# Kernel tuning notes

Measured on AMD Instinct MI355X. Metric: run time of the kernel, lower is better.

## Reference

```python
import jax, jax.numpy as jnp
import numpy as np

L = 4          # n_layers
HID = 64       # hidden_channels
MODES = 16     # n_modes
HEADS = 4      # n_heads
NP_SP = 500    # spatial engram patterns
NP_FR = 200    # spectral engram patterns
ED = 8         # embed_dim
WS = 4         # spatial window size
PRIME = 31.0


def setup_inputs() -> dict:
    key = jax.random.key(0)
    ks = jax.random.split(key, 20)
    B, Cin, Cout, S = 16, 3, 1, 16384
    f = lambda k, sh: jax.random.normal(k, sh, dtype=jnp.float32) * 0.05
    ch = HID // HEADS
    return {
        "x": jax.random.normal(ks[0], (B, Cin, S), dtype=jnp.float32),
        "lift_W": f(ks[1], (Cin, HID)), "lift_b": f(ks[2], (HID,)),
        "proj_W": f(ks[3], (HID, Cout)), "proj_b": f(ks[4], (Cout,)),
        "sp_emb": f(ks[5], (L, NP_SP, ED)), "sp_W": f(ks[6], (L, ED, HID)), "sp_b": f(ks[7], (L, HID)),
        "fr_emb": f(ks[8], (L, NP_FR, ED)), "fr_W": f(ks[9], (L, ED, HID * MODES)), "fr_b": f(ks[10], (L, HID * MODES)),
        "g_W1": f(ks[11], (L, 3 * HID, 64)), "g_b1": f(ks[12], (L, 64)),
        "g_W2": f(ks[13], (L, 64, 3)), "g_b2": f(ks[14], (L, 3)),
        "mhf_Wr": f(ks[15], (L, HEADS, ch, ch, MODES)),
        "mhf_Wi": f(ks[16], (L, HEADS, ch, ch, MODES)),
    }


def _spatial_engram(x, emb, W, b):
    # x: [B, C, S] -> hash each replicate-padded window of size WS -> embedding gather -> linear
    B, C, S = x.shape
    pad = WS // 2
    xp = jnp.pad(x, ((0, 0), (0, 0), (pad, pad)), mode='edge')   # [B, C, S+WS]
    sC = xp.sum(axis=1)                                          # [B, S+WS]
    # window sum over WS consecutive positions (vectorized over all seq positions)
    wsum = sC[:, 0:S] + sC[:, 1:S + 1] + sC[:, 2:S + 2] + sC[:, 3:S + 3]  # [B, S]
    idx = (wsum * PRIME).astype(jnp.int32) % NP_SP               # truncate-toward-zero like torch .long()
    idx = jnp.clip(idx, 0, NP_SP - 1)
    e = emb[idx]                                                 # [B, S, ED] gather
    out = e @ W + b                                              # [B, S, C]
    return out.transpose(0, 2, 1)                                # [B, C, S]


def _spectral_engram(x, emb, W, b):
    B, C, S = x.shape
    xf = jnp.fft.rfft(x, axis=-1)                                # [B, C, F]
    mag = jnp.abs(xf[:, :, :MODES]).mean(axis=1)                 # [B, MODES]
    idx = ((mag * 1000.0).astype(jnp.int32)).sum(axis=1) % NP_FR # [B]
    e = emb[idx]                                                 # [B, ED]
    proj = (e @ W + b).reshape(B, C, MODES)
    full = jnp.zeros((B, C, xf.shape[-1]), dtype=xf.dtype).at[:, :, :MODES].set(proj.astype(xf.dtype))
    return jnp.fft.irfft(full, n=S, axis=-1)


def _mhf_spectral_conv(x, Wr, Wi):
    # multi-head Fourier spectral conv: per-head complex channel mixing on low modes
    B, C, S = x.shape
    ch = C // HEADS
    xf = jnp.fft.rfft(x, axis=-1)                                # [B, C, F]
    xh = xf[:, :, :MODES].reshape(B, HEADS, ch, MODES)           # [B, H, ch, M]
    Wc = Wr + 1j * Wi                                            # [H, ch, ch, M]
    of = jnp.einsum('bhim,hiom->bhom', xh, Wc).reshape(B, C, MODES)
    full = jnp.zeros((B, C, xf.shape[-1]), dtype=xf.dtype).at[:, :, :MODES].set(of)
    return jnp.fft.irfft(full, n=S, axis=-1)


def _gated_fusion(sp, mh, fr, W1, b1, W2, b2):
    g = jnp.concatenate([sp.mean(-1), mh.mean(-1), fr.mean(-1)], axis=-1)  # [B, 3C]
    h = jax.nn.relu(g @ W1 + b1)
    w = jax.nn.softmax(h @ W2 + b2, axis=-1)                     # [B, 3]
    return (w[:, 0, None, None] * sp + w[:, 1, None, None] * mh + w[:, 2, None, None] * fr)


def reference(x, lift_W, lift_b, proj_W, proj_b, sp_emb, sp_W, sp_b,
              fr_emb, fr_W, fr_b, g_W1, g_b1, g_W2, g_b2, mhf_Wr, mhf_Wi):
    # lifting: [B, Cin, S] -> [B, HID, S]
    h = jnp.einsum('bcs,cd->bds', x, lift_W) + lift_b[None, :, None]
    for i in range(L):
        sp = _spatial_engram(h, sp_emb[i], sp_W[i], sp_b[i])
        mh = _mhf_spectral_conv(h, mhf_Wr[i], mhf_Wi[i])
        fr = _spectral_engram(h, fr_emb[i], fr_W[i], fr_b[i])
        h = _gated_fusion(sp, mh, fr, g_W1[i], g_b1[i], g_W2[i], g_b2[i])
        h = jax.nn.gelu(h, approximate=False)  # torch F.gelu default = exact erf
    out = jnp.einsum('bcs,cd->bds', h, proj_W) + proj_b[None, :, None]
    return out
```

## Files before the change

kernel.cpp:

```cpp
#include <hip/hip_runtime.h>
#include <math.h>

#define B_ 16
#define CIN_ 3
#define HID_ 64
#define S_ 16384
#define MODES_ 16
#define HEADS_ 4
#define CH_ 16
#define ED_ 8
#define NPSP_ 500
#define NPFR_ 200
#define LAYERS_ 4
#define RECW_ 42

__device__ __forceinline__ double gelu_exact(double v) {
    double y = v * 0.70710678118654752440;
    double t = y * y;
    double p = -1.2290555301717926e-09;
    p = fma(p, t, 1.4807192815879218e-08);
    p = fma(p, t, -1.6365838718281893e-07);
    p = fma(p, t, 1.6462114365889246e-06);
    p = fma(p, t, -1.4925650358406251e-05);
    p = fma(p, t, 1.2055332981789664e-04);
    p = fma(p, t, -8.5483270234508528e-04);
    p = fma(p, t, 5.2239776254421878e-03);
    p = fma(p, t, -2.6866170645131252e-02);
    p = fma(p, t, 1.1283791670955126e-01);
    p = fma(p, t, -3.7612638903183752e-01);
    p = fma(p, t, 1.1283791670955126e+00);
    double er = y * p;
    if (t > 0.5000001) er = erf(y);
    return 0.5 * v * (1.0 + er);
}

__device__ __constant__ double KC_[16] = {1.0, 0.99518472667219688624,
    0.98078528040323044913, 0.95694033573220886494, 0.92387953251128675613,
    0.88192126434835502971, 0.83146961230254523708, 0.77301045336273696081,
    0.70710678118654752440, 0.63439328416364549822, 0.55557023301960222474,
    0.47139673682599764856, 0.38268343236508977173, 0.29028467725446236764,
    0.19509032201612826785, 0.09801714032956060199};
__device__ __constant__ double KS_[16] = {0.0, 0.09801714032956060199,
    0.19509032201612826785, 0.29028467725446236764, 0.38268343236508977173,
    0.47139673682599764856, 0.55557023301960222474, 0.63439328416364549822,
    0.70710678118654752440, 0.77301045336273696081, 0.83146961230254523708,
    0.88192126434835502971, 0.92387953251128675613, 0.95694033573220886494,
    0.98078528040323044913, 0.99518472667219688624};

__global__ __launch_bounds__(256) void k_lift(const float* __restrict__ x,
                                              const float* __restrict__ W,
                                              const float* __restrict__ bias,
                                              float* __restrict__ h,
                                              double* __restrict__ sC2) {
    int b = blockIdx.y;
    int s = blockIdx.x * 256 + threadIdx.x;
    const float* xb = x + (size_t)b * CIN_ * S_ + s;
    double x0 = (double)xb[0];
    double x1 = (double)xb[S_];
    double x2 = (double)xb[2 * S_];
    float* hb = h + (size_t)b * HID_ * S_ + s;
    double accA = 0.0, accB = 0.0;
    for (int d = 0; d < HID_; ++d) {
        double v = x0 * (double)W[d];
        v = fma(x1, (double)W[HID_ + d], v);
        v = fma(x2, (double)W[2 * HID_ + d], v);
        v += (double)bias[d];
        hb[(size_t)d * S_] = (float)v;
        if (d < 32) accA += v; else accB += v;
    }
    sC2[(size_t)b * S_ + s] = accA;
    sC2[(size_t)(B_ + b) * S_ + s] = accB;
}

__global__ __launch_bounds__(256) void k_hash(const double* __restrict__ sC2,
                                              const float* __restrict__ emb_l,
                                              int* __restrict__ idx,
                                              double* __restrict__ Eb) {
    int b = blockIdx.y;
    int s0 = blockIdx.x * 256;
    int t = threadIdx.x;
    __shared__ double sl[260];
    for (int j = t; j < 260; j += 256) {
        int p = s0 - 2 + j;
        p = p < 0 ? 0 : (p > S_ - 1 ? S_ - 1 : p);
        sl[j] = sC2[(size_t)b * S_ + p] + sC2[(size_t)(B_ + b) * S_ + p];
    }
    __syncthreads();
    double wsum = ((sl[t] + sl[t + 1]) + sl[t + 2]) + sl[t + 3];
    int ti = (int)(wsum * 31.0);
    int id = ti % NPSP_;
    if (id < 0) id += NPSP_;
    idx[(size_t)b * S_ + s0 + t] = id;

    const float* er = emb_l + id * ED_;
    double ev[8];
#pragma unroll
    for (int k = 0; k < 8; k++) ev[k] = (double)er[k];

    int lane = t & 63, wv = t >> 6;
    __shared__ double red[4][8];
#pragma unroll
    for (int k = 0; k < 8; k++) {
        double v = ev[k];
        for (int off = 32; off > 0; off >>= 1) v += __shfl_down(v, off, 64);
        if (lane == 0) red[wv][k] = v;
    }
    __syncthreads();
    if (t < 8) {
        double v = red[0][t] + red[1][t] + red[2][t] + red[3][t];
        atomicAdd(&Eb[b * ED_ + t], v);
    }
}

__global__ __launch_bounds__(256, 2) void k_dft(const float* __restrict__ h,
                                                double* __restrict__ Xr,
                                                double* __restrict__ Xi) {
    int b = blockIdx.y;
    int c0 = blockIdx.x * 2;
    int t = threadIdx.x;
    const float* h0 = h + ((size_t)(b * HID_ + c0)) * S_ + t;
    const float* h1 = h0 + S_;

    double acc[64];
#pragma unroll
    for (int k = 0; k < 64; k++) acc[k] = 0.0;

    double cmv[16], smv[16];
    cmv[0] = 1.0; smv[0] = 0.0;
    cmv[1] = cospi((double)t / 8192.0);
    smv[1] = sinpi((double)t / 8192.0);
#pragma unroll
    for (int m = 2; m < 16; m++) {
        cmv[m] = cmv[m - 1] * cmv[1] - smv[m - 1] * smv[1];
        smv[m] = smv[m - 1] * cmv[1] + cmv[m - 1] * smv[1];
    }

    for (int k = 0; k < 16; k++) {
        int s = k << 8;
        double a0 = (double)h0[s];
        double b0 = (double)h0[s + 4096];
        double c0v = (double)h0[s + 8192];
        double d0 = (double)h0[s + 12288];
        double a1 = (double)h1[s];
        double b1 = (double)h1[s + 4096];
        double c1v = (double)h1[s + 8192];
        double d1 = (double)h1[s + 12288];

        double t10 = a0 + c0v, t20 = b0 + d0;
        double g00 = t10 + t20, g20 = t10 - t20;
        double ar0 = a0 - c0v, br0 = b0 - d0;
        double t11 = a1 + c1v, t21 = b1 + d1;
        double g01 = t11 + t21, g21 = t11 - t21;
        double ar1 = a1 - c1v, br1 = b1 - d1;

        acc[0] += g00;
        acc[32] += g01;
#pragma unroll
        for (int m = 1; m < 16; m++) {
            double c = cmv[m], s_ = smv[m];
            if ((m & 1) == 0) {
                double g0x = (m & 2) ? g20 : g00;
                double g1x = (m & 2) ? g21 : g01;
                acc[m]      = fma(g0x, c,  acc[m]);
                acc[16 + m] = fma(g0x, s_, acc[16 + m]);
                acc[32 + m] = fma(g1x, c,  acc[32 + m]);
                acc[48 + m] = fma(g1x, s_, acc[48 + m]);
            } else if ((m & 2) == 0) {
                acc[m]      = fma(ar0, c,  fma(-br0, s_, acc[m]));
                acc[16 + m] = fma(ar0, s_, fma( br0, c,  acc[16 + m]));
                acc[32 + m] = fma(ar1, c,  fma(-br1, s_, acc[32 + m]));
                acc[48 + m] = fma(ar1, s_, fma( br1, c,  acc[48 + m]));
            } else {
                acc[m]      = fma(ar0, c,  fma( br0, s_, acc[m]));
                acc[16 + m] = fma(ar0, s_, fma(-br0, c,  acc[16 + m]));
                acc[32 + m] = fma(ar1, c,  fma( br1, s_, acc[32 + m]));
                acc[48 + m] = fma(ar1, s_, fma(-br1, c,  acc[48 + m]));
            }
        }
#pragma unroll
        for (int m = 1; m < 16; m++) {
            double cn = cmv[m] * KC_[m] - smv[m] * KS_[m];
            double sn = smv[m] * KC_[m] + cmv[m] * KS_[m];
            cmv[m] = cn; smv[m] = sn;
        }
    }

    int lane = t & 63, wv = t >> 6;
    __shared__ double red[4][64];
#pragma unroll
    for (int k = 0; k < 64; k++) {
        double v = acc[k];
        for (int off = 32; off > 0; off >>= 1) v += __shfl_down(v, off, 64);
        if (lane == 0) red[wv][k] = v;
    }
    __syncthreads();
    if (t < 64) {
        double v = red[0][t] + red[1][t] + red[2][t] + red[3][t];
        int cc = t >> 5, im = (t >> 4) & 1, m = t & 15;
        size_t o = ((size_t)b * HID_ + c0 + cc) * MODES_ + m;
        if (im) Xi[o] = -v;
        else    Xr[o] = v;
    }
}

__global__ __launch_bounds__(256) void k_gate(const double* __restrict__ Xr,
                                              const double* __restrict__ Xi,
                                              const float* __restrict__ mWr,
                                              const float* __restrict__ mWi,
                                              const float* __restrict__ fr_emb_l,
                                              const float* __restrict__ fr_W_l,
                                              const float* __restrict__ fr_b_l,
                                              const double* __restrict__ Eb,
                                              const float* __restrict__ sp_W_l,
                                              const float* __restrict__ sp_b_l,
                                              const float* __restrict__ gW1,
                                              const float* __restrict__ gb1,
                                              const float* __restrict__ gW2,
                                              const float* __restrict__ gb2,
                                              double* __restrict__ RECg) {
    int b = blockIdx.x;
    int t = threadIdx.x;
    __shared__ double sXr[1024], sXi[1024];
    __shared__ double sMr[1024], sMi[1024], sP[1024];
    __shared__ double gg[192], h1s[64], sww[3];
    __shared__ int magI[MODES_];
    __shared__ int fidxS;

    for (int j = t; j < 1024; j += 256) {
        sXr[j] = Xr[(size_t)b * 1024 + j];
        sXi[j] = Xi[(size_t)b * 1024 + j];
    }
    __syncthreads();

    if (t < MODES_) {
        double acc = 0.0;
        for (int c = 0; c < HID_; c++) {
            double re = sXr[c * MODES_ + t];
            double im = sXi[c * MODES_ + t];
            acc += sqrt(re * re + im * im);
        }
        magI[t] = (int)(acc * (1.0 / 64.0) * 1000.0);
    }

    for (int u = t; u < 1024; u += 256) {
        int hh = u >> 8, rem = u & 255, o = rem >> 4, m = rem & 15;
        const float* wr = mWr + (size_t)hh * CH_ * CH_ * MODES_;
        const float* wi = mWi + (size_t)hh * CH_ * CH_ * MODES_;
        double aR = 0.0, aI = 0.0;
#pragma unroll 4
        for (int i = 0; i < CH_; i++) {
            double xrv = sXr[(hh * CH_ + i) * MODES_ + m];
            double xiv = sXi[(hh * CH_ + i) * MODES_ + m];
            double wrv = (double)wr[(i * CH_ + o) * MODES_ + m];
            double wiv = (double)wi[(i * CH_ + o) * MODES_ + m];
            aR += xrv * wrv - xiv * wiv;
            aI += xrv * wiv + xiv * wrv;
        }
        sMr[(hh * CH_ + o) * MODES_ + m] = aR;
        sMi[(hh * CH_ + o) * MODES_ + m] = aI;
    }
    __syncthreads();

    if (t == 0) {
        int ssum = 0;
        for (int m = 0; m < MODES_; m++) ssum += magI[m];
        int f = ssum % NPFR_;
        if (f < 0) f += NPFR_;
        fidxS = f;
    }
    __syncthreads();

    {
        const float* fe = fr_emb_l + fidxS * ED_;
        for (int u = t; u < 1024; u += 256) {
            double acc = 0.0;
            for (int e = 0; e < ED_; e++)
                acc += (double)fe[e] * (double)fr_W_l[e * 1024 + u];
            sP[u] = acc + (double)fr_b_l[u];
        }
    }
    __syncthreads();

    if (t < 64) {
        double a = 0.0;
        for (int e = 0; e < ED_; e++)
            a += Eb[b * ED_ + e] * (double)sp_W_l[e * 64 + t];
        gg[t]       = a * (1.0 / 16384.0) + (double)sp_b_l[t];
        gg[64 + t]  = sMr[t * MODES_] * (1.0 / 16384.0);
        gg[128 + t] = sP[t * MODES_] * (1.0 / 16384.0);
    }
    __syncthreads();
    if (t < 64) {
        double a = 0.0;
        for (int k = 0; k < 192; k++) a += gg[k] * (double)gW1[k * 64 + t];
        a += (double)gb1[t];
        h1s[t] = a > 0.0 ? a : 0.0;
    }
    __syncthreads();
    if (t == 0) {
        double l[3];
        for (int j = 0; j < 3; j++) {
            double a = 0.0;
            for (int k = 0; k < 64; k++) a += h1s[k] * (double)gW2[k * 3 + j];
            l[j] = a + (double)gb2[j];
        }
        double mx = fmax(l[0], fmax(l[1], l[2]));
        double e0 = exp(l[0] - mx), e1 = exp(l[1] - mx), e2 = exp(l[2] - mx);
        double sum = e0 + e1 + e2;
        sww[0] = e0 / sum; sww[1] = e1 / sum; sww[2] = e2 / sum;
    }
    __syncthreads();

    double w0s = sww[0], w1s = sww[1], w2s = sww[2];
    double* R = RECg + (size_t)b * HID_ * RECW_;
    for (int u = t; u < 1024; u += 256) {
        int c = u >> 4, m = u & 15;
        double km = (m == 0 ? 1.0 : 2.0) * (1.0 / 16384.0);
        R[c * RECW_ + 2 * m]     = km * (w1s * sMr[u] + w2s * sP[u]);
        R[c * RECW_ + 2 * m + 1] = (m == 0) ? 0.0 : -(km * w1s * sMi[u]);
    }
    for (int u = t; u < 512; u += 256) {
        int e = u >> 6, c = u & 63;
        R[c * RECW_ + 32 + e] = w0s * (double)sp_W_l[u];
    }
    if (t < 64) {
        R[t * RECW_ + 40] = w0s * (double)sp_b_l[t];
        R[t * RECW_ + 41] = 0.0;
    }
}

__global__ __launch_bounds__(256, 2) void k_recon(const int* __restrict__ idx,
                                                  const float* __restrict__ sp_emb_l,
                                                  const double* __restrict__ RECg,
                                                  float* __restrict__ h,
                                                  double* __restrict__ sC2) {
    int b = blockIdx.y;
    int cz = blockIdx.z;
    int cbase = cz * 32;
    int s0 = blockIdx.x * 256 + threadIdx.x;
    int t = threadIdx.x;
    __shared__ double rec[32 * RECW_];
    __shared__ float semb[NPSP_ * 9];
    for (int j = t; j < 32 * RECW_; j += 256)
        rec[j] = RECg[(size_t)b * HID_ * RECW_ + cbase * RECW_ + j];
    for (int j4 = t; j4 < NPSP_ * 2; j4 += 256) {
        float4 v = reinterpret_cast<const float4*>(sp_emb_l)[j4];
        int r = j4 >> 1, e0 = (j4 & 1) * 4;
        semb[r * 9 + e0]     = v.x;
        semb[r * 9 + e0 + 1] = v.y;
        semb[r * 9 + e0 + 2] = v.z;
        semb[r * 9 + e0 + 3] = v.w;
    }
    __syncthreads();

    int id0 = idx[(size_t)b * S_ + s0];
    int id1 = idx[(size_t)b * S_ + s0 + 4096];
    int id2 = idx[(size_t)b * S_ + s0 + 8192];
    int id3 = idx[(size_t)b * S_ + s0 + 12288];
    double e0v[8], e1v[8], e2v[8], e3v[8];
#pragma unroll
    for (int k = 0; k < 8; k++) {
        e0v[k] = (double)semb[id0 * 9 + k];
        e1v[k] = (double)semb[id1 * 9 + k];
        e2v[k] = (double)semb[id2 * 9 + k];
        e3v[k] = (double)semb[id3 * 9 + k];
    }

    double cb = cospi((double)s0 / 8192.0);
    double sb = sinpi((double)s0 / 8192.0);
    double cm[16], sm[16];
    cm[0] = 1.0; sm[0] = 0.0;
    cm[1] = cb;  sm[1] = sb;
#pragma unroll
    for (int m = 2; m < 16; m++) {
        cm[m] = cm[m - 1] * cb - sm[m - 1] * sb;
        sm[m] = sm[m - 1] * cb + cm[m - 1] * sb;
    }

    float* hb = h + (size_t)b * HID_ * S_ + (size_t)cbase * S_;
    double cs0 = 0.0, cs1 = 0.0, cs2 = 0.0, cs3 = 0.0;
    for (int c = 0; c < 32; c++) {
        const double2* r2 = (const double2*)(rec + c * RECW_);
        double base = rec[c * RECW_ + 40];
        double p0 = base, p1 = base, p2 = base, p3 = base;
#pragma unroll
        for (int k = 0; k < 4; k++) {
            double2 w = r2[16 + k];
            p0 = fma(e0v[2 * k], w.x, p0); p0 = fma(e0v[2 * k + 1], w.y, p0);
            p1 = fma(e1v[2 * k], w.x, p1); p1 = fma(e1v[2 * k + 1], w.y, p1);
            p2 = fma(e2v[2 * k], w.x, p2); p2 = fma(e2v[2 * k + 1], w.y, p2);
            p3 = fma(e3v[2 * k], w.x, p3); p3 = fma(e3v[2 * k + 1], w.y, p3);
        }
        double PA = 0.0, PB = 0.0, PC = 0.0, PD = 0.0, QB = 0.0, QD = 0.0;
#pragma unroll
        for (int mm = 0; mm < 16; mm += 4) {
            double2 q0 = r2[mm], q1 = r2[mm + 1], q2 = r2[mm + 2], q3 = r2[mm + 3];
            PA = fma(q0.x, cm[mm], PA);     PA = fma(q0.y, sm[mm], PA);
            PB = fma(q1.x, cm[mm + 1], PB); PB = fma(q1.y, sm[mm + 1], PB);
            QB = fma(q1.y, cm[mm + 1], QB); QB = fma(-q1.x, sm[mm + 1], QB);
            PC = fma(q2.x, cm[mm + 2], PC); PC = fma(q2.y, sm[mm + 2], PC);
            PD = fma(q3.x, cm[mm + 3], PD); PD = fma(q3.y, sm[mm + 3], PD);
            QD = fma(q3.y, cm[mm + 3], QD); QD = fma(-q3.x, sm[mm + 3], QD);
        }
        double u0 = PA + PC, u1 = PA - PC;
        double w0 = PB + PD, qd = QB - QD;
        double g0 = gelu_exact(p0 + (u0 + w0));
        double g1 = gelu_exact(p1 + (u1 + qd));
        double g2 = gelu_exact(p2 + (u0 - w0));
        double g3 = gelu_exact(p3 + (u1 - qd));
        hb[(size_t)c * S_ + s0]         = (float)g0;
        hb[(size_t)c * S_ + s0 + 4096]  = (float)g1;
        hb[(size_t)c * S_ + s0 + 8192]  = (float)g2;
        hb[(size_t)c * S_ + s0 + 12288] = (float)g3;
        cs0 += g0; cs1 += g1; cs2 += g2; cs3 += g3;
    }
    double* sc = sC2 + (size_t)(cz * B_ + b) * S_;
    sc[s0]         = cs0;
    sc[s0 + 4096]  = cs1;
    sc[s0 + 8192]  = cs2;
    sc[s0 + 12288] = cs3;
}

__global__ __launch_bounds__(256) void k_proj(const float* __restrict__ h,
                                              const float* __restrict__ pW,
                                              const float* __restrict__ pb,
                                              float* __restrict__ out) {
    int b = blockIdx.y;
    int s = blockIdx.x * 256 + threadIdx.x;
    const float* hb = h + (size_t)b * HID_ * S_ + s;
    double acc = 0.0;
    for (int d = 0; d < HID_; d++)
        acc += (double)hb[(size_t)d * S_] * (double)pW[d];
    out[(size_t)b * S_ + s] = (float)(acc + (double)pb[0]);
}

extern "C" void kernel_launch(void* const* d_in, const int* in_sizes, int n_in,
                              void* d_out, int out_size, void* d_ws, size_t ws_size,
                              hipStream_t stream) {
    const float* x      = (const float*)d_in[0];
    const float* lift_W = (const float*)d_in[1];
    const float* lift_b = (const float*)d_in[2];
    const float* proj_W = (const float*)d_in[3];
    const float* proj_b = (const float*)d_in[4];
    const float* sp_emb = (const float*)d_in[5];
    const float* sp_W   = (const float*)d_in[6];
    const float* sp_b   = (const float*)d_in[7];
    const float* fr_emb = (const float*)d_in[8];
    const float* fr_W   = (const float*)d_in[9];
    const float* fr_b   = (const float*)d_in[10];
    const float* g_W1   = (const float*)d_in[11];
    const float* g_b1   = (const float*)d_in[12];
    const float* g_W2   = (const float*)d_in[13];
    const float* g_b2   = (const float*)d_in[14];
    const float* mhf_Wr = (const float*)d_in[15];
    const float* mhf_Wi = (const float*)d_in[16];

    char* ws = (char*)d_ws;
    float* h    = (float*)ws;   ws += (size_t)B_ * HID_ * S_ * 4;
    double* sC2 = (double*)ws;  ws += (size_t)2 * B_ * S_ * 8;
    int* idx    = (int*)ws;     ws += (size_t)B_ * S_ * 4;
    double* Xr  = (double*)ws;  ws += (size_t)B_ * HID_ * MODES_ * 8;
    double* Xi  = (double*)ws;  ws += (size_t)B_ * HID_ * MODES_ * 8;
    double* REC = (double*)ws;  ws += (size_t)B_ * HID_ * RECW_ * 8;
    double* Eb  = (double*)ws;  ws += (size_t)LAYERS_ * B_ * ED_ * 8;

    hipMemsetAsync(Eb, 0, (size_t)LAYERS_ * B_ * ED_ * 8, stream);

    dim3 blk(256);
    k_lift<<<dim3(S_ / 256, B_), blk, 0, stream>>>(x, lift_W, lift_b, h, sC2);

    for (int lay = 0; lay < LAYERS_; ++lay) {
        k_hash<<<dim3(S_ / 256, B_), blk, 0, stream>>>(
            sC2, sp_emb + (size_t)lay * NPSP_ * ED_, idx, Eb + (size_t)lay * B_ * ED_);
        k_dft<<<dim3(HID_ / 2, B_), blk, 0, stream>>>(h, Xr, Xi);
        k_gate<<<dim3(B_), blk, 0, stream>>>(
            Xr, Xi,
            mhf_Wr + (size_t)lay * HEADS_ * CH_ * CH_ * MODES_,
            mhf_Wi + (size_t)lay * HEADS_ * CH_ * CH_ * MODES_,
            fr_emb + (size_t)lay * NPFR_ * ED_,
            fr_W + (size_t)lay * ED_ * HID_ * MODES_,
            fr_b + (size_t)lay * HID_ * MODES_,
            Eb + (size_t)lay * B_ * ED_,
            sp_W + (size_t)lay * ED_ * HID_,
            sp_b + (size_t)lay * HID_,
            g_W1 + (size_t)lay * 192 * 64,
            g_b1 + (size_t)lay * 64,
            g_W2 + (size_t)lay * 64 * 3,
            g_b2 + (size_t)lay * 3,
            REC);
        k_recon<<<dim3(S_ / 1024, B_, 2), blk, 0, stream>>>(
            idx, sp_emb + (size_t)lay * NPSP_ * ED_, REC, h, sC2);
    }

    k_proj<<<dim3(S_ / 256, B_), blk, 0, stream>>>(h, proj_W, proj_b, (float*)d_out);
}
```

Measured before the change: 569.0 us.

## Fuse hash into DFT kernel and split recon over four channel groups

Merges the spatial hash kernel into the DFT kernel as extra blocks in the same grid, so the two independent stages share one launch and run concurrently. The recon kernel now handles 16 channels per block across four z-slices instead of 32 across two, doubling its parallelism. Channel partial sums grow from two to four planes, so the hash step reads four buffers instead of two. The recon blocks now load the full embedding table into shared memory for half as many channels each, which adds redundant loads in exchange for more blocks.

After: 623.7 us. 1.1x slower.

```diff
diff --git a/kernel.cpp b/kernel.cpp
--- a/kernel.cpp
+++ b/kernel.cpp
@@ -51,7 +51,7 @@
                                               const float* __restrict__ W,
                                               const float* __restrict__ bias,
                                               float* __restrict__ h,
-                                              double* __restrict__ sC2) {
+                                              double* __restrict__ sC4) {
     int b = blockIdx.y;
     int s = blockIdx.x * 256 + threadIdx.x;
     const float* xb = x + (size_t)b * CIN_ * S_ + s;
@@ -59,147 +59,153 @@
     double x1 = (double)xb[S_];
     double x2 = (double)xb[2 * S_];
     float* hb = h + (size_t)b * HID_ * S_ + s;
-    double accA = 0.0, accB = 0.0;
+    double accs[4] = {0.0, 0.0, 0.0, 0.0};
     for (int d = 0; d < HID_; ++d) {
         double v = x0 * (double)W[d];
         v = fma(x1, (double)W[HID_ + d], v);
         v = fma(x2, (double)W[2 * HID_ + d], v);
         v += (double)bias[d];
         hb[(size_t)d * S_] = (float)v;
-        if (d < 32) accA += v; else accB += v;
-    }
-    sC2[(size_t)b * S_ + s] = accA;
-    sC2[(size_t)(B_ + b) * S_ + s] = accB;
-}
-
-__global__ __launch_bounds__(256) void k_hash(const double* __restrict__ sC2,
-                                              const float* __restrict__ emb_l,
-                                              int* __restrict__ idx,
-                                              double* __restrict__ Eb) {
+        accs[d >> 4] += v;
+    }
+#pragma unroll
+    for (int z = 0; z < 4; z++)
+        sC4[(size_t)(z * B_ + b) * S_ + s] = accs[z];
+}
+
+__global__ __launch_bounds__(256, 2) void k_dfthash(const float* __restrict__ h,
+                                                    double* __restrict__ Xr,
+                                                    double* __restrict__ Xi,
+                                                    const double* __restrict__ sC4,
+                                                    const float* __restrict__ emb_l,
+                                                    int* __restrict__ idx,
+                                                    double* __restrict__ Eb) {
     int b = blockIdx.y;
-    int s0 = blockIdx.x * 256;
     int t = threadIdx.x;
-    __shared__ double sl[260];
-    for (int j = t; j < 260; j += 256) {
-        int p = s0 - 2 + j;
-        p = p < 0 ? 0 : (p > S_ - 1 ? S_ - 1 : p);
-        sl[j] = sC2[(size_t)b * S_ + p] + sC2[(size_t)(B_ + b) * S_ + p];
-    }
-    __syncthreads();
-    double wsum = ((sl[t] + sl[t + 1]) + sl[t + 2]) + sl[t + 3];
-    int ti = (int)(wsum * 31.0);
-    int id = ti % NPSP_;
-    if (id < 0) id += NPSP_;
-    idx[(size_t)b * S_ + s0 + t] = id;
-
-    const float* er = emb_l + id * ED_;
-    double ev[8];
-#pragma unroll
-    for (int k = 0; k < 8; k++) ev[k] = (double)er[k];
-
-    int lane = t & 63, wv = t >> 6;
-    __shared__ double red[4][8];
-#pragma unroll
-    for (int k = 0; k < 8; k++) {
-        double v = ev[k];
-        for (int off = 32; off > 0; off >>= 1) v += __shfl_down(v, off, 64);
-        if (lane == 0) red[wv][k] = v;
-    }
-    __syncthreads();
-    if (t < 8) {
-        double v = red[0][t] + red[1][t] + red[2][t] + red[3][t];
-        atomicAdd(&Eb[b * ED_ + t], v);
-    }
-}
-
-__global__ __launch_bounds__(256, 2) void k_dft(const float* __restrict__ h,
-                                                double* __restrict__ Xr,
-                                                double* __restrict__ Xi) {
-    int b = blockIdx.y;
-    int c0 = blockIdx.x * 2;
-    int t = threadIdx.x;
-    const float* h0 = h + ((size_t)(b * HID_ + c0)) * S_ + t;
-    const float* h1 = h0 + S_;
-
-    double acc[64];
-#pragma unroll
-    for (int k = 0; k < 64; k++) acc[k] = 0.0;
-
-    double cmv[16], smv[16];
-    cmv[0] = 1.0; smv[0] = 0.0;
-    cmv[1] = cospi((double)t / 8192.0);
-    smv[1] = sinpi((double)t / 8192.0);
-#pragma unroll
-    for (int m = 2; m < 16; m++) {
-        cmv[m] = cmv[m - 1] * cmv[1] - smv[m - 1] * smv[1];
-        smv[m] = smv[m - 1] * cmv[1] + cmv[m - 1] * smv[1];
-    }
-
-    for (int k = 0; k < 16; k++) {
-        int s = k << 8;
-        double a0 = (double)h0[s];
-        double b0 = (double)h0[s + 4096];
-        double c0v = (double)h0[s + 8192];
-        double d0 = (double)h0[s + 12288];
-        double a1 = (double)h1[s];
-        double b1 = (double)h1[s + 4096];
-        double c1v = (double)h1[s + 8192];
-        double d1 = (double)h1[s + 12288];
-
-        double t10 = a0 + c0v, t20 = b0 + d0;
-        double g00 = t10 + t20, g20 = t10 - t20;
-        double ar0 = a0 - c0v, br0 = b0 - d0;
-        double t11 = a1 + c1v, t21 = b1 + d1;
-        double g01 = t11 + t21, g21 = t11 - t21;
-        double ar1 = a1 - c1v, br1 = b1 - d1;
-
-        acc[0] += g00;
-        acc[32] += g01;
-#pragma unroll
-        for (int m = 1; m < 16; m++) {
-            double c = cmv[m], s_ = smv[m];
-            if ((m & 1) == 0) {
-                double g0x = (m & 2) ? g20 : g00;
-                double g1x = (m & 2) ? g21 : g01;
-                acc[m]      = fma(g0x, c,  acc[m]);
-                acc[16 + m] = fma(g0x, s_, acc[16 + m]);
-                acc[32 + m] = fma(g1x, c,  acc[32 + m]);
-                acc[48 + m] = fma(g1x, s_, acc[48 + m]);
-            } else if ((m & 2) == 0) {
-                acc[m]      = fma(ar0, c,  fma(-br0, s_, acc[m]));
-                acc[16 + m] = fma(ar0, s_, fma( br0, c,  acc[16 + m]));
-                acc[32 + m] = fma(ar1, c,  fma(-br1, s_, acc[32 + m]));
-                acc[48 + m] = fma(ar1, s_, fma( br1, c,  acc[48 + m]));
-            } else {
-                acc[m]      = fma(ar0, c,  fma( br0, s_, acc[m]));
-                acc[16 + m] = fma(ar0, s_, fma(-br0, c,  acc[16 + m]));
-                acc[32 + m] = fma(ar1, c,  fma( br1, s_, acc[32 + m]));
-                acc[48 + m] = fma(ar1, s_, fma(-br1, c,  acc[48 + m]));
+    __shared__ double smem[292];
+
+    if (blockIdx.x < 32) {
+        int c0 = blockIdx.x * 2;
+        const float* h0 = h + ((size_t)(b * HID_ + c0)) * S_ + t;
+        const float* h1 = h0 + S_;
+
+        double acc[64];
+#pragma unroll
+        for (int k = 0; k < 64; k++) acc[k] = 0.0;
+
+        double cmv[16], smv[16];
+        cmv[0] = 1.0; smv[0] = 0.0;
+        cmv[1] = cospi((double)t / 8192.0);
+        smv[1] = sinpi((double)t / 8192.0);
+#pragma unroll
+        for (int m = 2; m < 16; m++) {
+            cmv[m] = cmv[m - 1] * cmv[1] - smv[m - 1] * smv[1];
+            smv[m] = smv[m - 1] * cmv[1] + cmv[m - 1] * smv[1];
+        }
+
+        for (int k = 0; k < 16; k++) {
+            int s = k << 8;
+            double a0 = (double)h0[s];
+            double b0 = (double)h0[s + 4096];
+            double c0v = (double)h0[s + 8192];
+            double d0 = (double)h0[s + 12288];
+            double a1 = (double)h1[s];
+            double b1 = (double)h1[s + 4096];
+            double c1v = (double)h1[s + 8192];
+            double d1 = (double)h1[s + 12288];
+
+            double t10 = a0 + c0v, t20 = b0 + d0;
+            double g00 = t10 + t20, g20 = t10 - t20;
+            double ar0 = a0 - c0v, br0 = b0 - d0;
+            double t11 = a1 + c1v, t21 = b1 + d1;
+            double g01 = t11 + t21, g21 = t11 - t21;
+            double ar1 = a1 - c1v, br1 = b1 - d1;
+
+            acc[0] += g00;
+            acc[32] += g01;
+#pragma unroll
+            for (int m = 1; m < 16; m++) {
+                double c = cmv[m], s_ = smv[m];
+                if ((m & 1) == 0) {
+                    double g0x = (m & 2) ? g20 : g00;
+                    double g1x = (m & 2) ? g21 : g01;
+                    acc[m]      = fma(g0x, c,  acc[m]);
+                    acc[16 + m] = fma(g0x, s_, acc[16 + m]);
+                    acc[32 + m] = fma(g1x, c,  acc[32 + m]);
+                    acc[48 + m] = fma(g1x, s_, acc[48 + m]);
+                } else if ((m & 2) == 0) {
+                    acc[m]      = fma(ar0, c,  fma(-br0, s_, acc[m]));
+                    acc[16 + m] = fma(ar0, s_, fma( br0, c,  acc[16 + m]));
+                    acc[32 + m] = fma(ar1, c,  fma(-br1, s_, acc[32 + m]));
+                    acc[48 + m] = fma(ar1, s_, fma( br1, c,  acc[48 + m]));
+                } else {
+                    acc[m]      = fma(ar0, c,  fma( br0, s_, acc[m]));
+                    acc[16 + m] = fma(ar0, s_, fma(-br0, c,  acc[16 + m]));
+                    acc[32 + m] = fma(ar1, c,  fma( br1, s_, acc[32 + m]));
+                    acc[48 + m] = fma(ar1, s_, fma(-br1, c,  acc[48 + m]));
+                }
             }
-        }
-#pragma unroll
-        for (int m = 1; m < 16; m++) {
-            double cn = cmv[m] * KC_[m] - smv[m] * KS_[m];
-            double sn = smv[m] * KC_[m] + cmv[m] * KS_[m];
-            cmv[m] = cn; smv[m] = sn;
-        }
-    }
-
-    int lane = t & 63, wv = t >> 6;
-    __shared__ double red[4][64];
-#pragma unroll
-    for (int k = 0; k < 64; k++) {
-        double v = acc[k];
-        for (int off = 32; off > 0; off >>= 1) v += __shfl_down(v, off, 64);
-        if (lane == 0) red[wv][k] = v;
-    }
-    __syncthreads();
-    if (t < 64) {
-        double v = red[0][t] + red[1][t] + red[2][t] + red[3][t];
-        int cc = t >> 5, im = (t >> 4) & 1, m = t & 15;
-        size_t o = ((size_t)b * HID_ + c0 + cc) * MODES_ + m;
-        if (im) Xi[o] = -v;
-        else    Xr[o] = v;
+#pragma unroll
+            for (int m = 1; m < 16; m++) {
+                double cn = cmv[m] * KC_[m] - smv[m] * KS_[m];
+                double sn = smv[m] * KC_[m] + cmv[m] * KS_[m];
+                cmv[m] = cn; smv[m] = sn;
+            }
+        }
+
+        int lane = t & 63, wv = t >> 6;
+        double* red = smem;
+#pragma unroll
+        for (int k = 0; k < 64; k++) {
+            double v = acc[k];
+            for (int off = 32; off > 0; off >>= 1) v += __shfl_down(v, off, 64);
+            if (lane == 0) red[wv * 64 + k] = v;
+        }
+        __syncthreads();
+        if (t < 64) {
+            double v = red[t] + red[64 + t] + red[128 + t] + red[192 + t];
+            int cc = t >> 5, im = (t >> 4) & 1, m = t & 15;
+            size_t o = ((size_t)b * HID_ + c0 + cc) * MODES_ + m;
+            if (im) Xi[o] = -v;
+            else    Xr[o] = v;
+        }
+    } else {
+        int s0 = (blockIdx.x - 32) * 256;
+        double* sl = smem;
+        double* red = smem + 260;
+        for (int j = t; j < 260; j += 256) {
+            int p = s0 - 2 + j;
+            p = p < 0 ? 0 : (p > S_ - 1 ? S_ - 1 : p);
+            double v = sC4[(size_t)b * S_ + p];
+            v += sC4[(size_t)(B_ + b) * S_ + p];
+            v += sC4[(size_t)(2 * B_ + b) * S_ + p];
+            v += sC4[(size_t)(3 * B_ + b) * S_ + p];
+            sl[j] = v;
+        }
+        __syncthreads();
+        double wsum = ((sl[t] + sl[t + 1]) + sl[t + 2]) + sl[t + 3];
+        int ti = (int)(wsum * 31.0);
+        int id = ti % NPSP_;
+        if (id < 0) id += NPSP_;
+        idx[(size_t)b * S_ + s0 + t] = id;
+
+        const float* er = emb_l + id * ED_;
+        double ev[8];
+#pragma unroll
+        for (int k = 0; k < 8; k++) ev[k] = (double)er[k];
+
+        int lane = t & 63, wv = t >> 6;
+#pragma unroll
+        for (int k = 0; k < 8; k++) {
+            double v = ev[k];
+            for (int off = 32; off > 0; off >>= 1) v += __shfl_down(v, off, 64);
+            if (lane == 0) red[wv * 8 + k] = v;
+        }
+        __syncthreads();
+        if (t < 8) {
+            double v = red[t] + red[8 + t] + red[16 + t] + red[24 + t];
+            atomicAdd(&Eb[b * ED_ + t], v);
+        }
     }
 }
 
@@ -333,15 +339,15 @@
                                                   const float* __restrict__ sp_emb_l,
                                                   const double* __restrict__ RECg,
                                                   float* __restrict__ h,
-                                                  double* __restrict__ sC2) {
+                                                  double* __restrict__ sC4) {
     int b = blockIdx.y;
     int cz = blockIdx.z;
-    int cbase = cz * 32;
+    int cbase = cz * 16;
     int s0 = blockIdx.x * 256 + threadIdx.x;
     int t = threadIdx.x;
-    __shared__ double rec[32 * RECW_];
+    __shared__ double rec[16 * RECW_];
     __shared__ float semb[NPSP_ * 9];
-    for (int j = t; j < 32 * RECW_; j += 256)
+    for (int j = t; j < 16 * RECW_; j += 256)
         rec[j] = RECg[(size_t)b * HID_ * RECW_ + cbase * RECW_ + j];
     for (int j4 = t; j4 < NPSP_ * 2; j4 += 256) {
         float4 v = reinterpret_cast<const float4*>(sp_emb_l)[j4];
@@ -379,7 +385,7 @@
 
     float* hb = h + (size_t)b * HID_ * S_ + (size_t)cbase * S_;
     double cs0 = 0.0, cs1 = 0.0, cs2 = 0.0, cs3 = 0.0;
-    for (int c = 0; c < 32; c++) {
+    for (int c = 0; c < 16; c++) {
         const double2* r2 = (const double2*)(rec + c * RECW_);
         double base = rec[c * RECW_ + 40];
         double p0 = base, p1 = base, p2 = base, p3 = base;
@@ -414,7 +420,7 @@
         hb[(size_t)c * S_ + s0 + 12288] = (float)g3;
         cs0 += g0; cs1 += g1; cs2 += g2; cs3 += g3;
     }
-    double* sc = sC2 + (size_t)(cz * B_ + b) * S_;
+    double* sc = sC4 + (size_t)(cz * B_ + b) * S_;
     sc[s0]         = cs0;
     sc[s0 + 4096]  = cs1;
     sc[s0 + 8192]  = cs2;
@@ -457,7 +463,7 @@
 
     char* ws = (char*)d_ws;
     float* h    = (float*)ws;   ws += (size_t)B_ * HID_ * S_ * 4;
-    double* sC2 = (double*)ws;  ws += (size_t)2 * B_ * S_ * 8;
+    double* sC4 = (double*)ws;  ws += (size_t)4 * B_ * S_ * 8;
     int* idx    = (int*)ws;     ws += (size_t)B_ * S_ * 4;
     double* Xr  = (double*)ws;  ws += (size_t)B_ * HID_ * MODES_ * 8;
     double* Xi  = (double*)ws;  ws += (size_t)B_ * HID_ * MODES_ * 8;
@@ -467,12 +473,12 @@
     hipMemsetAsync(Eb, 0, (size_t)LAYERS_ * B_ * ED_ * 8, stream);
 
     dim3 blk(256);
-    k_lift<<<dim3(S_ / 256, B_), blk, 0, stream>>>(x, lift_W, lift_b, h, sC2);
+    k_lift<<<dim3(S_ / 256, B_), blk, 0, stream>>>(x, lift_W, lift_b, h, sC4);
 
     for (int lay = 0; lay < LAYERS_; ++lay) {
-        k_hash<<<dim3(S_ / 256, B_), blk, 0, stream>>>(
-            sC2, sp_emb + (size_t)lay * NPSP_ * ED_, idx, Eb + (size_t)lay * B_ * ED_);
-        k_dft<<<dim3(HID_ / 2, B_), blk, 0, stream>>>(h, Xr, Xi);
+        k_dfthash<<<dim3(32 + 64, B_), blk, 0, stream>>>(
+            h, Xr, Xi, sC4, sp_emb + (size_t)lay * NPSP_ * ED_,
+            idx, Eb + (size_t)lay * B_ * ED_);
         k_gate<<<dim3(B_), blk, 0, stream>>>(
             Xr, Xi,
             mhf_Wr + (size_t)lay * HEADS_ * CH_ * CH_ * MODES_,
@@ -488,8 +494,8 @@
             g_W2 + (size_t)lay * 64 * 3,
             g_b2 + (size_t)lay * 3,
             REC);
-        k_recon<<<dim3(S_ / 1024, B_, 2), blk, 0, stream>>>(
-            idx, sp_emb + (size_t)lay * NPSP_ * ED_, REC, h, sC2);
+        k_recon<<<dim3(S_ / 1024, B_, 4), blk, 0, stream>>>(
+            idx, sp_emb + (size_t)lay * NPSP_ * ED_, REC, h, sC4);
     }
 
     k_proj<<<dim3(S_ / 256, B_), blk, 0, stream>>>(h, proj_W, proj_b, (float*)d_out);
```
